# Optimization experiments

Measured on AMD Instinct MI355X. Metric: run time of the kernel, lower is better.

## Reference

```python
import jax, jax.numpy as jnp
import numpy as np

N_NODES = 100000
EPS = 1e-12


def _sage_conv(x, src, dst, Wl, bl, Wr):
    # PyG SAGEConv (aggr='mean'): lin_l(mean of neighbor msgs) + lin_r(x)
    msgs = x[src]                                                # [E, d] gather
    agg = jax.ops.segment_sum(msgs, dst, num_segments=N_NODES)  # [N, d] scatter-add
    deg = jax.ops.segment_sum(jnp.ones((src.shape[0],), x.dtype), dst,
                              num_segments=N_NODES)             # [N]
    agg = agg / jnp.maximum(deg, 1.0)[:, None]                  # scatter-mean
    return agg @ Wl + bl + x @ Wr


def setup_inputs() -> dict:
    key = jax.random.key(0)
    ks = jax.random.split(key, 16)
    d_in, d_h = 64, 64
    E = 1600000
    s = 0.1
    inp = {
        'x': jax.random.normal(ks[0], (N_NODES, d_in), jnp.float32),
        'edge_index': jax.random.randint(ks[1], (2, E), 0, N_NODES, jnp.int64),
    }
    dims = [(d_in, d_h), (d_h, d_h), (d_h, d_h), (d_h, d_h)]
    for i, (di, do) in enumerate(dims, start=1):
        inp[f'Wl{i}'] = s * jax.random.normal(ks[3 * i - 1], (di, do), jnp.float32)
        inp[f'bl{i}'] = jnp.zeros((do,), jnp.float32)
        inp[f'Wr{i}'] = s * jax.random.normal(ks[3 * i], (di, do), jnp.float32)
    return inp


def reference(x, edge_index, Wl1, bl1, Wr1, Wl2, bl2, Wr2, Wl3, bl3, Wr3, Wl4, bl4, Wr4):
    src, dst = edge_index[0], edge_index[1]
    # dropout is identity in eval mode
    h1 = jax.nn.relu(_sage_conv(x, src, dst, Wl1, bl1, Wr1))
    h2 = jax.nn.relu(_sage_conv(h1, src, dst, Wl2, bl2, Wr2)) + h1
    h3 = jax.nn.relu(_sage_conv(h2, src, dst, Wl3, bl3, Wr3)) + h2
    out = _sage_conv(h3, src, dst, Wl4, bl4, Wr4)
    # F.normalize(p=2, dim=1, eps=1e-12)
    norm = jnp.maximum(jnp.linalg.norm(out, axis=1, keepdims=True), EPS)
    return out / norm
```

## Files before the change

kernel.cpp:

```cpp
#include <hip/hip_runtime.h>


#include <hip/hip_bf16.h>

static inline size_t al256(size_t x) { return (x + 255) & ~(size_t)255; }

#define EPB 8192

typedef _Float16 f16x8 __attribute__((ext_vector_type(8)));
typedef float f32x4 __attribute__((ext_vector_type(4)));

__global__ void k_detect(const unsigned int* __restrict__ raw, int E, int* __restrict__ flag) {
  int nz = 0;
#pragma unroll
  for (int k = 0; k < 64; ++k) {
    int i = threadIdx.x + (k << 8);
    if (i < E && raw[2 * (size_t)i + 1] != 0u) nz = 1;
  }
  unsigned long long b = __ballot(nz != 0);
  if ((threadIdx.x & 63) == 0 && b) atomicOr(flag, 1);
}

__global__ __launch_bounds__(256) void k_bcount(const unsigned int* __restrict__ raw, int E,
                                                int span, const int* __restrict__ flag,
                                                int* __restrict__ bucketCount) {
  __shared__ int lh[256];
  int t = threadIdx.x;
  lh[t] = 0;
  __syncthreads();
  int f = *flag;
  int base = blockIdx.x * EPB;
#pragma unroll 4
  for (int k = 0; k < EPB / 256; ++k) {
    int i = base + k * 256 + t;
    if (i < E) {
      int dst = f ? (int)raw[E + i] : (int)raw[2 * (size_t)(E + i)];
      atomicAdd(&lh[dst / span], 1);
    }
  }
  __syncthreads();
  int c = lh[t];
  if (c) atomicAdd(&bucketCount[t], c);
}

__global__ void k_bscan(const int* __restrict__ bucketCount, int* __restrict__ boff,
                        int* __restrict__ cursorB, int* __restrict__ rs, int N, int E) {
  __shared__ int sa[256], sb[256];
  int t = threadIdx.x;
  int v = bucketCount[t];
  sa[t] = v;
  __syncthreads();
  int* s = sa;
  int* d = sb;
  for (int off = 1; off < 256; off <<= 1) {
    d[t] = s[t] + (t >= off ? s[t - off] : 0);
    __syncthreads();
    int* tmp = s; s = d; d = tmp;
  }
  int inc = s[t];
  int ex = inc - v;
  boff[t] = ex;
  cursorB[t] = ex;
  if (t == 255) boff[256] = inc;
  if (t == 0) rs[N] = E;
}

__global__ __launch_bounds__(256) void k_bscatter(const unsigned int* __restrict__ raw, int E,
                                                  int span, const int* __restrict__ flag,
                                                  int* __restrict__ cursorB,
                                                  unsigned* __restrict__ bdata) {
  __shared__ int lh[256], lcur[256], gbase[256];
  int t = threadIdx.x;
  lh[t] = 0;
  lcur[t] = 0;
  __syncthreads();
  int f = *flag;
  int base = blockIdx.x * EPB;
#pragma unroll 4
  for (int k = 0; k < EPB / 256; ++k) {
    int i = base + k * 256 + t;
    if (i < E) {
      int dst = f ? (int)raw[E + i] : (int)raw[2 * (size_t)(E + i)];
      atomicAdd(&lh[dst / span], 1);
    }
  }
  __syncthreads();
  int c = lh[t];
  gbase[t] = c ? atomicAdd(&cursorB[t], c) : 0;
  __syncthreads();
#pragma unroll 4
  for (int k = 0; k < EPB / 256; ++k) {
    int i = base + k * 256 + t;
    if (i < E) {
      int s_, d_;
      if (f) { s_ = (int)raw[i]; d_ = (int)raw[E + i]; }
      else   { s_ = (int)raw[2 * (size_t)i]; d_ = (int)raw[2 * (size_t)(E + i)]; }
      int b = d_ / span;
      int pos = atomicAdd(&lcur[b], 1);
      bdata[(size_t)gbase[b] + pos] = ((unsigned)(d_ - b * span) << 17) | (unsigned)s_;
    }
  }
}

__global__ __launch_bounds__(256) void k_bbuild(const unsigned* __restrict__ bdata,
                                                const int* __restrict__ boff, int span, int N,
                                                int* __restrict__ csr, int* __restrict__ rs,
                                                float* __restrict__ invdeg) {
  __shared__ int cnt[512], sa[512], sb[512], cur[512];
  int b = blockIdx.x;
  int t = threadIdx.x;
  int node0 = b * span;
  int beg = boff[b], end = boff[b + 1];
  cnt[t] = 0;
  cnt[t + 256] = 0;
  __syncthreads();
  for (int i = beg + t; i < end; i += 256) {
    atomicAdd(&cnt[bdata[i] >> 17], 1);
  }
  __syncthreads();
  sa[t] = cnt[t];
  sa[t + 256] = cnt[t + 256];
  __syncthreads();
  int* s = sa;
  int* d = sb;
  for (int off = 1; off < 512; off <<= 1) {
    d[t] = s[t] + (t >= off ? s[t - off] : 0);
    int i2 = t + 256;
    d[i2] = s[i2] + (i2 >= off ? s[i2 - off] : 0);
    __syncthreads();
    int* tmp = s; s = d; d = tmp;
  }
  int ex0 = s[t] - cnt[t];
  int ex1 = s[t + 256] - cnt[t + 256];
  cur[t] = ex0;
  cur[t + 256] = ex1;
  if (t < span) {
    int node = node0 + t;
    if (node < N) {
      rs[node] = beg + ex0;
      invdeg[node] = 1.0f / fmaxf((float)cnt[t], 1.0f);
    }
  }
  int t2 = t + 256;
  if (t2 < span) {
    int node = node0 + t2;
    if (node < N) {
      rs[node] = beg + ex1;
      invdeg[node] = 1.0f / fmaxf((float)cnt[t2], 1.0f);
    }
  }
  __syncthreads();
  for (int i = beg + t; i < end; i += 256) {
    unsigned p = bdata[i];
    int pos = atomicAdd(&cur[p >> 17], 1);
    csr[beg + pos] = (int)(p & 0x1FFFFu);
  }
}

template <int IT>
__global__ __launch_bounds__(256) void k_gemm(
    const void* __restrict__ hv_, const float* __restrict__ Wl,
    const float* __restrict__ Wr, const float* __restrict__ bl,
    unsigned short* __restrict__ Pf, unsigned short* __restrict__ R16, int n) {
  __shared__ uint4 hAu[512];
  char* hAraw = (char*)hAu;
  int t = threadIdx.x;
  int n0 = blockIdx.x * 64;
  int w = t >> 6;
  int l = t & 63;
  int lo16 = l & 15;
  int g = l >> 4;

#pragma unroll
  for (int c = 0; c < 4; ++c) {
    int idx = t + c * 256;
    int row = idx >> 4;
    int fc = idx & 15;
    int nn = n0 + row;
    uint2 u = make_uint2(0u, 0u);
    if (nn < n) {
      if (IT == 0) {
        const float* h = (const float*)hv_;
        float4 hv = *(const float4*)&h[(size_t)nn * 64 + fc * 4];
        union { _Float16 p[4]; uint2 u; } cv;
        cv.p[0] = (_Float16)hv.x; cv.p[1] = (_Float16)hv.y;
        cv.p[2] = (_Float16)hv.z; cv.p[3] = (_Float16)hv.w;
        u = cv.u;
      } else {
        u = *(const uint2*)((const char*)hv_ + (size_t)nn * 128 + fc * 8);
      }
    }
    int byte = (row * 128 + fc * 8) ^ ((row & 7) << 4);
    *(uint2*)(hAraw + byte) = u;
  }

  const float* Wsel = (w < 2) ? Wl : Wr;
  int colbase = (w & 1) * 32;
  f16x8 bfr[2][2];
#pragma unroll
  for (int nf = 0; nf < 2; ++nf) {
    int j = colbase + nf * 16 + lo16;
#pragma unroll
    for (int kk = 0; kk < 2; ++kk) {
      int k0 = kk * 32 + g * 8;
      f16x8 bb;
#pragma unroll
      for (int s = 0; s < 8; ++s) bb[s] = (_Float16)Wsel[(k0 + s) * 64 + j];
      bfr[nf][kk] = bb;
    }
  }
  __syncthreads();

  f32x4 acc[4][2];
#pragma unroll
  for (int mf = 0; mf < 4; ++mf)
#pragma unroll
    for (int nf = 0; nf < 2; ++nf) acc[mf][nf] = (f32x4){0.f, 0.f, 0.f, 0.f};

#pragma unroll
  for (int mf = 0; mf < 4; ++mf) {
    int row = mf * 16 + lo16;
    int swz = (row & 7) << 4;
    f16x8 av0 = *(const f16x8*)(hAraw + row * 128 + ((g * 16) ^ swz));
    f16x8 av1 = *(const f16x8*)(hAraw + row * 128 + ((64 + g * 16) ^ swz));
#pragma unroll
    for (int nf = 0; nf < 2; ++nf) {
      acc[mf][nf] = __builtin_amdgcn_mfma_f32_16x16x32_f16(av0, bfr[nf][0], acc[mf][nf], 0, 0, 0);
      acc[mf][nf] = __builtin_amdgcn_mfma_f32_16x16x32_f16(av1, bfr[nf][1], acc[mf][nf], 0, 0, 0);
    }
  }

#pragma unroll
  for (int nf = 0; nf < 2; ++nf) {
    int col = colbase + nf * 16 + lo16;
    float bv = (w >= 2) ? bl[col] : 0.f;
#pragma unroll
    for (int mf = 0; mf < 4; ++mf) {
#pragma unroll
      for (int r = 0; r < 4; ++r) {
        int grow = n0 + mf * 16 + g * 4 + r;
        if (grow < n) {
          float v = acc[mf][nf][r];
          union { _Float16 hh; unsigned short us; } cv;
          if (w < 2) {
            cv.hh = (_Float16)v;
            Pf[(size_t)grow * 64 + col] = cv.us;
          } else {
            cv.hh = (_Float16)(v + bv);
            R16[(size_t)grow * 64 + col] = cv.us;
          }
        }
      }
    }
  }
}

template <int MODE>
__global__ __launch_bounds__(256) void k_gather(
    const uint2* __restrict__ P2, const unsigned short* __restrict__ R16,
    const unsigned short* __restrict__ hres, const int* __restrict__ csr,
    const int* __restrict__ rs, const float* __restrict__ invdeg,
    void* __restrict__ hout, int n) {
  typedef _Float16 h2 __attribute__((ext_vector_type(2)));
  union HU { unsigned u32; h2 h; };
  union Q4 { uint2 u; _Float16 hh[4]; };
  int l = threadIdx.x & 63;
  int v = (blockIdx.x << 2) + (threadIdx.x >> 6);
  if (v >= n) return;
  int q = l & 15;
  int g = l >> 4;
  int beg = rs[v], end = rs[v + 1];
  float idg = invdeg[v];
  Q4 rq;
  rq.u = *(const uint2*)((const char*)R16 + (size_t)v * 128 + q * 8);
  Q4 hq;
  hq.u = make_uint2(0u, 0u);
  if (MODE == 1) hq.u = *(const uint2*)((const char*)hres + (size_t)v * 128 + q * 8);

  float s0 = 0.f, s1 = 0.f, s2 = 0.f, s3 = 0.f;
  int i = beg;
  int rem = end - beg;
  int myidx = 0;
  if (rem > 0) myidx = csr[i + (q < rem ? q : (rem - 1))];
  for (; i + 16 <= end;) {
    int inext = i + 16;
    int remn = end - inext;
    int nxt = 0;
    if (remn > 0) nxt = csr[inext + (q < remn ? q : (remn - 1))];
    h2 a0 = (h2)0, a1 = (h2)0;
#pragma unroll
    for (int t = 0; t < 4; ++t) {
      int sel = __shfl(myidx, 4 * t + g, 64);
      uint2 u = P2[(unsigned)((sel << 4) + q)];
      HU b0, b1;
      b0.u32 = u.x;
      b1.u32 = u.y;
      a0 += b0.h;
      a1 += b1.h;
    }
    s0 += (float)a0[0];
    s1 += (float)a0[1];
    s2 += (float)a1[0];
    s3 += (float)a1[1];
    myidx = nxt;
    i = inext;
  }
  int r = end - i;
  if (r > 0) {
    h2 a0 = (h2)0, a1 = (h2)0;
#pragma unroll
    for (int t = 0; t < 4; ++t) {
      if (4 * t >= r) break;
      int e = 4 * t + g;
      int sel = __shfl(myidx, e < r ? e : 0, 64);
      if (e < r) {
        uint2 u = P2[(unsigned)((sel << 4) + q)];
        HU b0, b1;
        b0.u32 = u.x;
        b1.u32 = u.y;
        a0 += b0.h;
        a1 += b1.h;
      }
    }
    s0 += (float)a0[0];
    s1 += (float)a0[1];
    s2 += (float)a1[0];
    s3 += (float)a1[1];
  }
  s0 += __shfl_xor(s0, 16, 64); s0 += __shfl_xor(s0, 32, 64);
  s1 += __shfl_xor(s1, 16, 64); s1 += __shfl_xor(s1, 32, 64);
  s2 += __shfl_xor(s2, 16, 64); s2 += __shfl_xor(s2, 32, 64);
  s3 += __shfl_xor(s3, 16, 64); s3 += __shfl_xor(s3, 32, 64);

  if (l < 16) {
    float4 o;
    o.x = s0 * idg + (float)rq.hh[0];
    o.y = s1 * idg + (float)rq.hh[1];
    o.z = s2 * idg + (float)rq.hh[2];
    o.w = s3 * idg + (float)rq.hh[3];
    if (MODE == 0) {
      o.x = fmaxf(o.x, 0.f); o.y = fmaxf(o.y, 0.f);
      o.z = fmaxf(o.z, 0.f); o.w = fmaxf(o.w, 0.f);
    } else if (MODE == 1) {
      o.x = fmaxf(o.x, 0.f) + (float)hq.hh[0];
      o.y = fmaxf(o.y, 0.f) + (float)hq.hh[1];
      o.z = fmaxf(o.z, 0.f) + (float)hq.hh[2];
      o.w = fmaxf(o.w, 0.f) + (float)hq.hh[3];
    } else {
      float sq = o.x * o.x + o.y * o.y + o.z * o.z + o.w * o.w;
#pragma unroll
      for (int m = 1; m < 16; m <<= 1) sq += __shfl_xor(sq, m, 64);
      float nrm = fmaxf(sqrtf(sq), 1e-12f);
      o.x /= nrm; o.y /= nrm; o.z /= nrm; o.w /= nrm;
    }
    if (MODE == 2) {
      *(float4*)&((float*)hout)[((size_t)v << 6) + (q << 2)] = o;
    } else {
      Q4 oq;
      oq.hh[0] = (_Float16)o.x; oq.hh[1] = (_Float16)o.y;
      oq.hh[2] = (_Float16)o.z; oq.hh[3] = (_Float16)o.w;
      *(uint2*)((char*)hout + (size_t)v * 128 + q * 8) = oq.u;
    }
  }
}

extern "C" void kernel_launch(void* const* d_in, const int* in_sizes, int n_in,
                              void* d_out, int out_size, void* d_ws, size_t ws_size,
                              hipStream_t stream) {
  const float* x = (const float*)d_in[0];
  const unsigned int* eraw = (const unsigned int*)d_in[1];
  const float* Wl[4] = {(const float*)d_in[2], (const float*)d_in[5],
                        (const float*)d_in[8], (const float*)d_in[11]};
  const float* blv[4] = {(const float*)d_in[3], (const float*)d_in[6],
                         (const float*)d_in[9], (const float*)d_in[12]};
  const float* Wr[4] = {(const float*)d_in[4], (const float*)d_in[7],
                        (const float*)d_in[10], (const float*)d_in[13]};
  const int N = in_sizes[0] / 64;
  const int E = in_sizes[1] / 2;
  const int span = (N + 255) / 256;
  float* out = (float*)d_out;

  char* w = (char*)d_ws;
  size_t off = 0;
  int* flag = (int*)(w + off);        off = al256(off + 4);
  int* bucketCount = (int*)(w + off); off = al256(off + 256 * 4);
  int* boff = (int*)(w + off);        off = al256(off + 257 * 4);
  int* cursorB = (int*)(w + off);     off = al256(off + 256 * 4);
  int* csr = (int*)(w + off);         off = al256(off + (size_t)E * 4);
  float* invdeg = (float*)(w + off);  off = al256(off + (size_t)N * 4);
  int* rs = (int*)(w + off);          off = al256(off + (size_t)(N + 1) * 4);
  unsigned* bdata = (unsigned*)(w + off); off = al256(off + (size_t)E * 4);
  unsigned short* hA = (unsigned short*)(w + off); off = al256(off + (size_t)N * 64 * 2);
  unsigned short* hB = (unsigned short*)(w + off); off = al256(off + (size_t)N * 64 * 2);
  unsigned short* Pf = (unsigned short*)(w + off); off = al256(off + (size_t)N * 64 * 2);
  unsigned short* R16 = (unsigned short*)(w + off); off = al256(off + (size_t)N * 64 * 2);

  hipMemsetAsync(flag, 0, 4, stream);
  hipMemsetAsync(bucketCount, 0, 256 * 4, stream);

  int eb = (E + EPB - 1) / EPB;
  k_detect<<<1, 256, 0, stream>>>(eraw, E, flag);
  k_bcount<<<eb, 256, 0, stream>>>(eraw, E, span, flag, bucketCount);
  k_bscan<<<1, 256, 0, stream>>>(bucketCount, boff, cursorB, rs, N, E);
  k_bscatter<<<eb, 256, 0, stream>>>(eraw, E, span, flag, cursorB, bdata);
  k_bbuild<<<256, 256, 0, stream>>>(bdata, boff, span, N, csr, rs, invdeg);

  int gb = (N + 63) / 64;
  int nb4 = (N + 3) / 4;
  const uint2* P2 = (const uint2*)Pf;
  k_gemm<0><<<gb, 256, 0, stream>>>(x, Wl[0], Wr[0], blv[0], Pf, R16, N);
  k_gather<0><<<nb4, 256, 0, stream>>>(P2, R16, nullptr, csr, rs, invdeg, hA, N);
  k_gemm<1><<<gb, 256, 0, stream>>>(hA, Wl[1], Wr[1], blv[1], Pf, R16, N);
  k_gather<1><<<nb4, 256, 0, stream>>>(P2, R16, hA, csr, rs, invdeg, hB, N);
  k_gemm<1><<<gb, 256, 0, stream>>>(hB, Wl[2], Wr[2], blv[2], Pf, R16, N);
  k_gather<1><<<nb4, 256, 0, stream>>>(P2, R16, hB, csr, rs, invdeg, hA, N);
  k_gemm<1><<<gb, 256, 0, stream>>>(hA, Wl[3], Wr[3], blv[3], Pf, R16, N);
  k_gather<2><<<nb4, 256, 0, stream>>>(P2, R16, nullptr, csr, rs, invdeg, out, N);
}
```

Before: 318.1 us.

## Process two nodes per wavefront in neighbor gather kernel

The gather kernel now assigns two destination nodes to each 64-lane wavefront, 32 lanes per node, instead of one node per wave. Each half handles two edges per step rather than four, and the loop runs to the larger of the two degrees, with masking for the shorter one. The aim is to cut per-wave overhead and fit mean degree 16 better. It loses the software prefetch of the next CSR index block, and divergent degrees waste lanes.

```diff
diff --git a/kernel.cpp b/kernel.cpp
--- a/kernel.cpp
+++ b/kernel.cpp
@@ -8,7 +8,10 @@
 #define EPB 8192
 
 typedef _Float16 f16x8 __attribute__((ext_vector_type(8)));
+typedef _Float16 h2v __attribute__((ext_vector_type(2)));
 typedef float f32x4 __attribute__((ext_vector_type(4)));
+union HU { unsigned u32; h2v h; };
+union Q4 { uint2 u; _Float16 hh[4]; };
 
 __global__ void k_detect(const unsigned int* __restrict__ raw, int E, int* __restrict__ flag) {
   int nz = 0;
@@ -256,45 +259,51 @@
 }
 
 template <int MODE>
-__global__ __launch_bounds__(256) void k_gather(
+__global__ __launch_bounds__(256) void k_gatherP(
     const uint2* __restrict__ P2, const unsigned short* __restrict__ R16,
     const unsigned short* __restrict__ hres, const int* __restrict__ csr,
     const int* __restrict__ rs, const float* __restrict__ invdeg,
-    void* __restrict__ hout, int n) {
-  typedef _Float16 h2 __attribute__((ext_vector_type(2)));
-  union HU { unsigned u32; h2 h; };
-  union Q4 { uint2 u; _Float16 hh[4]; };
-  int l = threadIdx.x & 63;
-  int v = (blockIdx.x << 2) + (threadIdx.x >> 6);
-  if (v >= n) return;
+    void* __restrict__ hout, int n, int E) {
+  int t = threadIdx.x;
+  int w = t >> 6;
+  int l = t & 63;
+  int half = l >> 5;
   int q = l & 15;
-  int g = l >> 4;
-  int beg = rs[v], end = rs[v + 1];
-  float idg = invdeg[v];
-  Q4 rq;
-  rq.u = *(const uint2*)((const char*)R16 + (size_t)v * 128 + q * 8);
-  Q4 hq;
-  hq.u = make_uint2(0u, 0u);
-  if (MODE == 1) hq.u = *(const uint2*)((const char*)hres + (size_t)v * 128 + q * 8);
-
+  int g2 = (l >> 4) & 1;
+  int v = blockIdx.x * 8 + w * 2 + half;
+  int bH = rs[v < n ? v : n];
+  int eH = rs[(v + 1) < n ? (v + 1) : n];
+  int rH = eH - bH;
+  float idg = 1.f;
+  Q4 rq; rq.u = make_uint2(0u, 0u);
+  Q4 hq; hq.u = make_uint2(0u, 0u);
+  if ((l & 16) == 0 && v < n) {
+    idg = invdeg[v];
+    rq.u = *(const uint2*)((const char*)R16 + (size_t)v * 128 + q * 8);
+    if (MODE == 1) hq.u = *(const uint2*)((const char*)hres + (size_t)v * 128 + q * 8);
+  }
   float s0 = 0.f, s1 = 0.f, s2 = 0.f, s3 = 0.f;
-  int i = beg;
-  int rem = end - beg;
-  int myidx = 0;
-  if (rem > 0) myidx = csr[i + (q < rem ? q : (rem - 1))];
-  for (; i + 16 <= end;) {
-    int inext = i + 16;
-    int remn = end - inext;
-    int nxt = 0;
-    if (remn > 0) nxt = csr[inext + (q < remn ? q : (remn - 1))];
-    h2 a0 = (h2)0, a1 = (h2)0;
-#pragma unroll
-    for (int t = 0; t < 4; ++t) {
-      int sel = __shfl(myidx, 4 * t + g, 64);
+  int rOther = __shfl_xor(rH, 32, 64);
+  int maxR = rH > rOther ? rH : rOther;
+  int nb = (maxR + 15) >> 4;
+  for (int bt = 0; bt < nb; ++bt) {
+    int rem = rH - (bt << 4);
+    int offc = (rem > 0) ? ((q < rem) ? q : rem - 1) : 0;
+    int addr = bH + (bt << 4) + offc;
+    addr = (addr < E) ? addr : E - 1;
+    int myidx = csr[addr];
+    h2v a0 = (h2v)0, a1 = (h2v)0;
+    int remMax = maxR - (bt << 4);
+#pragma unroll
+    for (int tt = 0; tt < 8; ++tt) {
+      if (2 * tt >= remMax) break;
+      int ee = 2 * tt + g2;
+      int sel = __shfl(myidx, (half << 5) + ee, 64);
       uint2 u = P2[(unsigned)((sel << 4) + q)];
+      bool m = ee < rem;
       HU b0, b1;
-      b0.u32 = u.x;
-      b1.u32 = u.y;
+      b0.u32 = m ? u.x : 0u;
+      b1.u32 = m ? u.y : 0u;
       a0 += b0.h;
       a1 += b1.h;
     }
@@ -302,37 +311,13 @@
     s1 += (float)a0[1];
     s2 += (float)a1[0];
     s3 += (float)a1[1];
-    myidx = nxt;
-    i = inext;
-  }
-  int r = end - i;
-  if (r > 0) {
-    h2 a0 = (h2)0, a1 = (h2)0;
-#pragma unroll
-    for (int t = 0; t < 4; ++t) {
-      if (4 * t >= r) break;
-      int e = 4 * t + g;
-      int sel = __shfl(myidx, e < r ? e : 0, 64);
-      if (e < r) {
-        uint2 u = P2[(unsigned)((sel << 4) + q)];
-        HU b0, b1;
-        b0.u32 = u.x;
-        b1.u32 = u.y;
-        a0 += b0.h;
-        a1 += b1.h;
-      }
-    }
-    s0 += (float)a0[0];
-    s1 += (float)a0[1];
-    s2 += (float)a1[0];
-    s3 += (float)a1[1];
-  }
-  s0 += __shfl_xor(s0, 16, 64); s0 += __shfl_xor(s0, 32, 64);
-  s1 += __shfl_xor(s1, 16, 64); s1 += __shfl_xor(s1, 32, 64);
-  s2 += __shfl_xor(s2, 16, 64); s2 += __shfl_xor(s2, 32, 64);
-  s3 += __shfl_xor(s3, 16, 64); s3 += __shfl_xor(s3, 32, 64);
-
-  if (l < 16) {
+  }
+  s0 += __shfl_xor(s0, 16, 64);
+  s1 += __shfl_xor(s1, 16, 64);
+  s2 += __shfl_xor(s2, 16, 64);
+  s3 += __shfl_xor(s3, 16, 64);
+
+  if ((l & 16) == 0 && v < n) {
     float4 o;
     o.x = s0 * idg + (float)rq.hh[0];
     o.y = s1 * idg + (float)rq.hh[1];
@@ -406,14 +391,14 @@
   k_bbuild<<<256, 256, 0, stream>>>(bdata, boff, span, N, csr, rs, invdeg);
 
   int gb = (N + 63) / 64;
-  int nb4 = (N + 3) / 4;
+  int nb8 = (N + 7) / 8;
   const uint2* P2 = (const uint2*)Pf;
   k_gemm<0><<<gb, 256, 0, stream>>>(x, Wl[0], Wr[0], blv[0], Pf, R16, N);
-  k_gather<0><<<nb4, 256, 0, stream>>>(P2, R16, nullptr, csr, rs, invdeg, hA, N);
+  k_gatherP<0><<<nb8, 256, 0, stream>>>(P2, R16, nullptr, csr, rs, invdeg, hA, N, E);
   k_gemm<1><<<gb, 256, 0, stream>>>(hA, Wl[1], Wr[1], blv[1], Pf, R16, N);
-  k_gather<1><<<nb4, 256, 0, stream>>>(P2, R16, hA, csr, rs, invdeg, hB, N);
+  k_gatherP<1><<<nb8, 256, 0, stream>>>(P2, R16, hA, csr, rs, invdeg, hB, N, E);
   k_gemm<1><<<gb, 256, 0, stream>>>(hB, Wl[2], Wr[2], blv[2], Pf, R16, N);
-  k_gather<1><<<nb4, 256, 0, stream>>>(P2, R16, hB, csr, rs, invdeg, hA, N);
+  k_gatherP<1><<<nb8, 256, 0, stream>>>(P2, R16, hB, csr, rs, invdeg, hA, N, E);
   k_gemm<1><<<gb, 256, 0, stream>>>(hA, Wl[3], Wr[3], blv[3], Pf, R16, N);
-  k_gather<2><<<nb4, 256, 0, stream>>>(P2, R16, nullptr, csr, rs, invdeg, out, N);
-}
+  k_gatherP<2><<<nb8, 256, 0, stream>>>(P2, R16, nullptr, csr, rs, invdeg, out, N, E);
+}
```

New measurement: 333.3 us. 4.8% more time.
